# Performance work log

Hardware: AMD Instinct MI355X
Metric: run time of the kernel (lower is better)

Reference implementation:

```python
import jax, jax.numpy as jnp
import numpy as np

N, E, DI, DO = 100000, 1600000, 64, 64
EPS = 1e-6


def setup_inputs() -> dict:
    key = jax.random.key(0)
    k1, k2, k3, k4 = jax.random.split(key, 4)
    x = jax.random.normal(k1, (N, DI), dtype=jnp.float32)
    src = jax.random.randint(k2, (E,), 0, N, dtype=jnp.int64)
    tgt = jax.random.randint(k3, (E,), 0, N, dtype=jnp.int64)
    kf, kw = jax.random.split(k4)
    # Xavier-uniform init, torch Linear layout: W [out, in]
    limf = float(np.sqrt(6.0 / (2 * DI + DO)))
    limw = float(np.sqrt(6.0 / (2 * DI + 1)))
    Wf = jax.random.uniform(kf, (DO, 2 * DI), jnp.float32, -limf, limf)
    bf = jnp.zeros((DO,), jnp.float32)
    Ww = jax.random.uniform(kw, (1, 2 * DI), jnp.float32, -limw, limw)
    bw = jnp.zeros((1,), jnp.float32)
    return {"x": x, "Wf": Wf, "bf": bf, "Ww": Ww, "bw": bw,
            "src": src, "tgt": tgt, "num_nodes": N}


def reference(x, Wf, bf, Ww, bw, src, tgt, num_nodes):
    # gather endpoints and build edge features [E, 2*di]
    h = jnp.concatenate([x[src], x[tgt]], axis=1)
    y = jax.nn.relu(h @ Wf.T + bf)            # [E, do]
    a = h @ Ww.T + bw                          # [E, 1]
    # global (all-edge) max for numerical stability, as in the original
    a_exp = jnp.exp(a - jnp.max(a, axis=0, keepdims=True))
    # Mtgt @ v  ==  segment_sum(v, tgt)
    a_sum = jax.ops.segment_sum(a_exp, tgt, num_segments=num_nodes) + EPS  # [N, 1]
    o = jax.ops.segment_sum(y * a_exp, tgt, num_segments=num_nodes) / a_sum  # [N, do]
    return o
```

## Files before the change

kernel.cpp:

```cpp
#include <hip/hip_runtime.h>
#include <math.h>


#define DID 64
#define DOD 64
#define SCAN_CHUNK 1024

__device__ __forceinline__ unsigned f2key(float f) {
  unsigned u = __float_as_uint(f);
  return (u & 0x80000000u) ? ~u : (u | 0x80000000u);
}
__device__ __forceinline__ float key2f(unsigned k) {
  unsigned u = (k & 0x80000000u) ? (k ^ 0x80000000u) : ~k;
  return __uint_as_float(u);
}

__global__ __launch_bounds__(256) void node_uv_kernel(
    const float* __restrict__ x, const float* __restrict__ Wf,
    const float* __restrict__ Ww, int N,
    float* __restrict__ u, float* __restrict__ v,
    float* __restrict__ p, float* __restrict__ q,
    unsigned* __restrict__ pqmax_key) {
  const int lane = threadIdx.x & 63;
  float wa[64], wb[64];
  const float4* wr = (const float4*)(Wf + (size_t)lane * 128);
  #pragma unroll
  for (int k4 = 0; k4 < 16; ++k4) {
    float4 t = wr[k4];
    wa[k4 * 4 + 0] = t.x; wa[k4 * 4 + 1] = t.y;
    wa[k4 * 4 + 2] = t.z; wa[k4 * 4 + 3] = t.w;
  }
  #pragma unroll
  for (int k4 = 0; k4 < 16; ++k4) {
    float4 t = wr[16 + k4];
    wb[k4 * 4 + 0] = t.x; wb[k4 * 4 + 1] = t.y;
    wb[k4 * 4 + 2] = t.z; wb[k4 * 4 + 3] = t.w;
  }
  const float wsl = Ww[lane];
  const float wtl = Ww[64 + lane];

  const int wid = blockIdx.x * (blockDim.x >> 6) + (threadIdx.x >> 6);
  const int nw  = gridDim.x * (blockDim.x >> 6);
  float pmax = -INFINITY, qmax = -INFINITY;
  for (int n = wid; n < N; n += nw) {
    float xl = x[(size_t)n * DID + lane];
    float pp = xl * wsl, qq = xl * wtl;
    #pragma unroll
    for (int o = 32; o >= 1; o >>= 1) {
      pp += __shfl_xor(pp, o);
      qq += __shfl_xor(qq, o);
    }
    pmax = fmaxf(pmax, pp);
    qmax = fmaxf(qmax, qq);
    float uu = 0.f, vv = 0.f;
    #pragma unroll
    for (int k = 0; k < 64; ++k) {
      float xb = __shfl(xl, k);
      uu = fmaf(xb, wa[k], uu);
      vv = fmaf(xb, wb[k], vv);
    }
    u[(size_t)n * DOD + lane] = uu;
    v[(size_t)n * DOD + lane] = vv;
    if (lane == 0) { p[n] = pp; q[n] = qq; }
  }
  if (lane == 0) {
    atomicMax(&pqmax_key[0], f2key(pmax));
    atomicMax(&pqmax_key[1], f2key(qmax));
  }
}

__global__ __launch_bounds__(256) void hist_kernel(
    const int* __restrict__ tgt, int E, int* __restrict__ hist) {
  int tid = blockIdx.x * blockDim.x + threadIdx.x;
  int st  = gridDim.x * blockDim.x;
  int e4  = E >> 2;
  const int4* t4p = (const int4*)tgt;
  for (int i = tid; i < e4; i += st) {
    int4 t4 = t4p[i];
    atomicAdd(&hist[t4.x], 1);
    atomicAdd(&hist[t4.y], 1);
    atomicAdd(&hist[t4.z], 1);
    atomicAdd(&hist[t4.w], 1);
  }
  for (int e = (e4 << 2) + tid; e < E; e += st) atomicAdd(&hist[tgt[e]], 1);
}

__global__ __launch_bounds__(256) void scan1_kernel(
    const int* __restrict__ hist, int* __restrict__ rowstart,
    int* __restrict__ bsum, int N) {
  int base = blockIdx.x * SCAN_CHUNK + threadIdx.x * 4;
  int h[4]; int ts = 0;
  #pragma unroll
  for (int j = 0; j < 4; ++j) {
    int i = base + j;
    h[j] = (i < N) ? hist[i] : 0;
    ts += h[j];
  }
  int lane = threadIdx.x & 63, wv = threadIdx.x >> 6;
  int sc = ts;
  #pragma unroll
  for (int o = 1; o < 64; o <<= 1) {
    int t = __shfl_up(sc, o);
    if (lane >= o) sc += t;
  }
  __shared__ int wtot[4];
  if (lane == 63) wtot[wv] = sc;
  __syncthreads();
  int woff = 0;
  for (int w = 0; w < wv; ++w) woff += wtot[w];
  int excl = woff + sc - ts;
  #pragma unroll
  for (int j = 0; j < 4; ++j) {
    int i = base + j;
    if (i < N) rowstart[i] = excl;
    excl += h[j];
  }
  if (threadIdx.x == 0) {
    int tot = 0;
    for (int w = 0; w < 4; ++w) tot += wtot[w];
    bsum[blockIdx.x] = tot;
  }
}

__global__ __launch_bounds__(256) void scan2_kernel(int* __restrict__ bsum, int SB) {
  __shared__ int tmp[256];
  int t = threadIdx.x;
  int s = (t < SB) ? bsum[t] : 0;
  tmp[t] = s;
  __syncthreads();
  int acc = s;
  for (int o = 1; o < 256; o <<= 1) {
    int vv = (t >= o) ? tmp[t - o] : 0;
    __syncthreads();
    acc += vv;
    tmp[t] = acc;
    __syncthreads();
  }
  if (t < SB) bsum[t] = acc - s;
}

__global__ __launch_bounds__(256) void scan3_kernel(
    int* __restrict__ rowstart, int* __restrict__ cursor,
    const int* __restrict__ bsum, int N, int E) {
  int base = blockIdx.x * SCAN_CHUNK + threadIdx.x * 4;
  int off = bsum[blockIdx.x];
  #pragma unroll
  for (int j = 0; j < 4; ++j) {
    int i = base + j;
    if (i < N) {
      int r = rowstart[i] + off;
      rowstart[i] = r;
      cursor[i] = r;
    }
  }
  if (blockIdx.x == 0 && threadIdx.x == 0) rowstart[N] = E;
}

__global__ __launch_bounds__(256) void fill_kernel(
    const int* __restrict__ src, const int* __restrict__ tgt,
    const float* __restrict__ p, const float* __restrict__ q,
    const unsigned* __restrict__ pqmax_key, int E,
    int* __restrict__ cursor, int2* __restrict__ csr,
    unsigned* __restrict__ wmax_key) {
  const float M = key2f(pqmax_key[0]) + key2f(pqmax_key[1]);
  int tid = blockIdx.x * blockDim.x + threadIdx.x;
  int st  = gridDim.x * blockDim.x;
  int e4  = E >> 2;
  const int4* s4p = (const int4*)src;
  const int4* t4p = (const int4*)tgt;
  float wm = 0.f;
  for (int i = tid; i < e4; i += st) {
    int4 s4 = s4p[i], t4 = t4p[i];
    float a0 = p[s4.x] + q[t4.x];
    float a1 = p[s4.y] + q[t4.y];
    float a2 = p[s4.z] + q[t4.z];
    float a3 = p[s4.w] + q[t4.w];
    float w0 = __expf(a0 - M), w1 = __expf(a1 - M);
    float w2 = __expf(a2 - M), w3 = __expf(a3 - M);
    wm = fmaxf(wm, fmaxf(fmaxf(w0, w1), fmaxf(w2, w3)));
    int p0 = atomicAdd(&cursor[t4.x], 1);
    int p1 = atomicAdd(&cursor[t4.y], 1);
    int p2 = atomicAdd(&cursor[t4.z], 1);
    int p3 = atomicAdd(&cursor[t4.w], 1);
    csr[p0] = make_int2(s4.x, __float_as_int(w0));
    csr[p1] = make_int2(s4.y, __float_as_int(w1));
    csr[p2] = make_int2(s4.z, __float_as_int(w2));
    csr[p3] = make_int2(s4.w, __float_as_int(w3));
  }
  for (int e = (e4 << 2) + tid; e < E; e += st) {
    int t = tgt[e], s = src[e];
    float w = __expf(p[s] + q[t] - M);
    wm = fmaxf(wm, w);
    int pos = atomicAdd(&cursor[t], 1);
    csr[pos] = make_int2(s, __float_as_int(w));
  }
  #pragma unroll
  for (int o = 32; o >= 1; o >>= 1) wm = fmaxf(wm, __shfl_xor(wm, o));
  if ((threadIdx.x & 63) == 0) atomicMax(wmax_key, f2key(wm));
}

__global__ __launch_bounds__(256) void gather_kernel(
    const int* __restrict__ rowstart, const int2* __restrict__ csr,
    const float* __restrict__ u, const float* __restrict__ v,
    const float* __restrict__ bf, const unsigned* __restrict__ wmax_key,
    int N, float* __restrict__ o) {
  const int lane = threadIdx.x & 63;
  const float bfl = bf[lane];
  const float epsEff = 1e-6f * key2f(*wmax_key);
  const int wid = blockIdx.x * (blockDim.x >> 6) + (threadIdx.x >> 6);
  const int nw  = gridDim.x * (blockDim.x >> 6);
  for (int n = wid; n < N; n += nw) {
    const int beg = rowstart[n], end = rowstart[n + 1];
    const float vtl = v[(size_t)n * DOD + lane];
    float acc = 0.f, wl = 0.f;
    for (int bb = beg; bb < end; bb += 64) {
      const int idx = bb + lane;
      int2 c = make_int2(0, 0);
      if (idx < end) c = csr[idx];
      float cw = __uint_as_float((unsigned)c.y);
      wl += cw;
      const int cnt4 = (min(64, end - bb) + 3) & ~3;
      for (int j = 0; j < cnt4; j += 4) {
        int s0 = __shfl(c.x, j + 0), s1 = __shfl(c.x, j + 1);
        int s2 = __shfl(c.x, j + 2), s3 = __shfl(c.x, j + 3);
        float w0 = __shfl(cw, j + 0), w1 = __shfl(cw, j + 1);
        float w2 = __shfl(cw, j + 2), w3 = __shfl(cw, j + 3);
        float r0 = u[(size_t)s0 * DOD + lane];
        float r1 = u[(size_t)s1 * DOD + lane];
        float r2 = u[(size_t)s2 * DOD + lane];
        float r3 = u[(size_t)s3 * DOD + lane];
        acc = fmaf(fmaxf(r0 + vtl + bfl, 0.f), w0, acc);
        acc = fmaf(fmaxf(r1 + vtl + bfl, 0.f), w1, acc);
        acc = fmaf(fmaxf(r2 + vtl + bfl, 0.f), w2, acc);
        acc = fmaf(fmaxf(r3 + vtl + bfl, 0.f), w3, acc);
      }
    }
    #pragma unroll
    for (int off = 32; off >= 1; off >>= 1) wl += __shfl_xor(wl, off);
    o[(size_t)n * DOD + lane] = acc / (wl + epsEff);
  }
}

extern "C" void kernel_launch(void* const* d_in, const int* in_sizes, int n_in,
                              void* d_out, int out_size, void* d_ws, size_t ws_size,
                              hipStream_t stream) {
  const float* x  = (const float*)d_in[0];
  const float* Wf = (const float*)d_in[1];
  const float* bf = (const float*)d_in[2];
  const float* Ww = (const float*)d_in[3];
  const int* src = (const int*)d_in[5];
  const int* tgt = (const int*)d_in[6];

  const int N = in_sizes[0] / DID;
  const int E = in_sizes[5];

  int2*  csr = (int2*)d_ws;
  float* u   = (float*)(csr + E);
  float* v   = u + (size_t)N * DOD;
  float* p   = v + (size_t)N * DOD;
  float* q   = p + N;
  int* hist     = (int*)(q + N);
  int* rowstart = hist + N;
  int* cursor   = rowstart + N + 1;
  int* bsum     = cursor + N;
  unsigned* pqmax_key = (unsigned*)(bsum + 256);
  unsigned* wmax_key  = pqmax_key + 2;

  hipMemsetAsync(hist, 0, (size_t)N * sizeof(int), stream);
  hipMemsetAsync(pqmax_key, 0, 3 * sizeof(unsigned), stream);

  const int SB = (N + SCAN_CHUNK - 1) / SCAN_CHUNK;

  node_uv_kernel<<<1024, 256, 0, stream>>>(x, Wf, Ww, N, u, v, p, q, pqmax_key);
  hist_kernel<<<1024, 256, 0, stream>>>(tgt, E, hist);
  scan1_kernel<<<SB, 256, 0, stream>>>(hist, rowstart, bsum, N);
  scan2_kernel<<<1, 256, 0, stream>>>(bsum, SB);
  scan3_kernel<<<SB, 256, 0, stream>>>(rowstart, cursor, bsum, N, E);
  fill_kernel<<<1024, 256, 0, stream>>>(src, tgt, p, q, pqmax_key, E, cursor,
                                        csr, wmax_key);
  gather_kernel<<<2048, 256, 0, stream>>>(rowstart, csr, u, v, bf, wmax_key,
                                          N, (float*)d_out);
}
```

Baseline: 481.5 us.

## Rewrite node projection as shared-memory tiled GEMM with register blocking

```diff
diff --git a/kernel.cpp b/kernel.cpp
--- a/kernel.cpp
+++ b/kernel.cpp
@@ -5,6 +5,9 @@
 #define DID 64
 #define DOD 64
 #define SCAN_CHUNK 1024
+#define TN 128
+#define LDA 129
+#define LDB 129
 
 __device__ __forceinline__ unsigned f2key(float f) {
   unsigned u = __float_as_uint(f);
@@ -15,55 +18,112 @@
   return __uint_as_float(u);
 }
 
-__global__ __launch_bounds__(256) void node_uv_kernel(
+__global__ __launch_bounds__(256, 2) void node_uv_kernel(
     const float* __restrict__ x, const float* __restrict__ Wf,
     const float* __restrict__ Ww, int N,
     float* __restrict__ u, float* __restrict__ v,
     float* __restrict__ p, float* __restrict__ q,
     unsigned* __restrict__ pqmax_key) {
-  const int lane = threadIdx.x & 63;
-  float wa[64], wb[64];
-  const float4* wr = (const float4*)(Wf + (size_t)lane * 128);
-  #pragma unroll
-  for (int k4 = 0; k4 < 16; ++k4) {
-    float4 t = wr[k4];
-    wa[k4 * 4 + 0] = t.x; wa[k4 * 4 + 1] = t.y;
-    wa[k4 * 4 + 2] = t.z; wa[k4 * 4 + 3] = t.w;
-  }
-  #pragma unroll
-  for (int k4 = 0; k4 < 16; ++k4) {
-    float4 t = wr[16 + k4];
-    wb[k4 * 4 + 0] = t.x; wb[k4 * 4 + 1] = t.y;
-    wb[k4 * 4 + 2] = t.z; wb[k4 * 4 + 3] = t.w;
-  }
-  const float wsl = Ww[lane];
-  const float wtl = Ww[64 + lane];
-
-  const int wid = blockIdx.x * (blockDim.x >> 6) + (threadIdx.x >> 6);
-  const int nw  = gridDim.x * (blockDim.x >> 6);
+  __shared__ float xT[64 * LDA];
+  __shared__ float wT[64 * LDB];
+  __shared__ float Wsv[128];
+
+  const int tid = threadIdx.x;
+
+  {
+    const float4* wf4 = (const float4*)Wf;
+    for (int f4 = tid; f4 < 64 * 32; f4 += 256) {
+      int j = f4 >> 5, c4 = (f4 & 31) << 2;
+      float4 t = wf4[f4];
+      float tv[4] = {t.x, t.y, t.z, t.w};
+      #pragma unroll
+      for (int ci = 0; ci < 4; ++ci) {
+        int c = c4 + ci;
+        int k  = (c < 64) ? c : (c - 64);
+        int jj = (c < 64) ? j : (64 + j);
+        wT[k * LDB + jj] = tv[ci];
+      }
+    }
+    if (tid < 128) Wsv[tid] = Ww[tid];
+  }
+
   float pmax = -INFINITY, qmax = -INFINITY;
-  for (int n = wid; n < N; n += nw) {
-    float xl = x[(size_t)n * DID + lane];
-    float pp = xl * wsl, qq = xl * wtl;
+
+  const int tn = tid >> 4;
+  const int tj = tid & 15;
+  const int n0 = tn * 8, j0 = tj * 8;
+  const int ntiles = (N + TN - 1) / TN;
+
+  for (int tile = blockIdx.x; tile < ntiles; tile += gridDim.x) {
+    const int base = tile * TN;
+    __syncthreads();
+    {
+      const float4* x4 = (const float4*)(x + (size_t)base * DID);
+      for (int f4 = tid; f4 < TN * 16; f4 += 256) {
+        int n = f4 >> 4, k4 = (f4 & 15) << 2;
+        float4 t = (base + n < N) ? x4[f4] : make_float4(0.f, 0.f, 0.f, 0.f);
+        xT[(k4 + 0) * LDA + n] = t.x;
+        xT[(k4 + 1) * LDA + n] = t.y;
+        xT[(k4 + 2) * LDA + n] = t.z;
+        xT[(k4 + 3) * LDA + n] = t.w;
+      }
+    }
+    __syncthreads();
+
+    float acc[8][8];
     #pragma unroll
-    for (int o = 32; o >= 1; o >>= 1) {
-      pp += __shfl_xor(pp, o);
-      qq += __shfl_xor(qq, o);
-    }
-    pmax = fmaxf(pmax, pp);
-    qmax = fmaxf(qmax, qq);
-    float uu = 0.f, vv = 0.f;
+    for (int i = 0; i < 8; ++i)
+      #pragma unroll
+      for (int jx = 0; jx < 8; ++jx) acc[i][jx] = 0.f;
+
+    #pragma unroll 4
+    for (int k = 0; k < 64; ++k) {
+      float4 a0 = *(const float4*)&xT[k * LDA + n0];
+      float4 a1 = *(const float4*)&xT[k * LDA + n0 + 4];
+      float4 b0 = *(const float4*)&wT[k * LDB + j0];
+      float4 b1 = *(const float4*)&wT[k * LDB + j0 + 4];
+      float av[8] = {a0.x, a0.y, a0.z, a0.w, a1.x, a1.y, a1.z, a1.w};
+      float bv[8] = {b0.x, b0.y, b0.z, b0.w, b1.x, b1.y, b1.z, b1.w};
+      #pragma unroll
+      for (int i = 0; i < 8; ++i)
+        #pragma unroll
+        for (int jx = 0; jx < 8; ++jx)
+          acc[i][jx] = fmaf(av[i], bv[jx], acc[i][jx]);
+    }
+
     #pragma unroll
-    for (int k = 0; k < 64; ++k) {
-      float xb = __shfl(xl, k);
-      uu = fmaf(xb, wa[k], uu);
-      vv = fmaf(xb, wb[k], vv);
-    }
-    u[(size_t)n * DOD + lane] = uu;
-    v[(size_t)n * DOD + lane] = vv;
-    if (lane == 0) { p[n] = pp; q[n] = qq; }
-  }
-  if (lane == 0) {
+    for (int i = 0; i < 8; ++i) {
+      int n = base + n0 + i;
+      if (n < N) {
+        float* dst = (j0 < 64) ? (u + (size_t)n * DOD + j0)
+                               : (v + (size_t)n * DOD + (j0 - 64));
+        *(float4*)dst       = make_float4(acc[i][0], acc[i][1], acc[i][2], acc[i][3]);
+        *(float4*)(dst + 4) = make_float4(acc[i][4], acc[i][5], acc[i][6], acc[i][7]);
+      }
+    }
+
+    if (tid < TN) {
+      int n = base + tid;
+      if (n < N) {
+        float pp = 0.f, qq = 0.f;
+        #pragma unroll 8
+        for (int k = 0; k < 64; ++k) {
+          float xv = xT[k * LDA + tid];
+          pp = fmaf(xv, Wsv[k], pp);
+          qq = fmaf(xv, Wsv[64 + k], qq);
+        }
+        p[n] = pp; q[n] = qq;
+        pmax = fmaxf(pmax, pp); qmax = fmaxf(qmax, qq);
+      }
+    }
+  }
+
+  #pragma unroll
+  for (int o = 32; o >= 1; o >>= 1) {
+    pmax = fmaxf(pmax, __shfl_xor(pmax, o));
+    qmax = fmaxf(qmax, __shfl_xor(qmax, o));
+  }
+  if ((tid & 63) == 0) {
     atomicMax(&pqmax_key[0], f2key(pmax));
     atomicMax(&pqmax_key[1], f2key(qmax));
   }
@@ -270,8 +330,9 @@
   hipMemsetAsync(pqmax_key, 0, 3 * sizeof(unsigned), stream);
 
   const int SB = (N + SCAN_CHUNK - 1) / SCAN_CHUNK;
-
-  node_uv_kernel<<<1024, 256, 0, stream>>>(x, Wf, Ww, N, u, v, p, q, pqmax_key);
+  const int ntiles = (N + TN - 1) / TN;
+
+  node_uv_kernel<<<ntiles, 256, 0, stream>>>(x, Wf, Ww, N, u, v, p, q, pqmax_key);
   hist_kernel<<<1024, 256, 0, stream>>>(tgt, E, hist);
   scan1_kernel<<<SB, 256, 0, stream>>>(hist, rowstart, bsum, N);
   scan2_kernel<<<1, 256, 0, stream>>>(bsum, SB);
```

New measurement: 435.0 us. 9.7% less time.
